# Kernel optimization log

Measured on AMD Instinct MI355X. Metric: run time of the kernel, lower is better.

Reference implementation:

```python
import jax, jax.numpy as jnp
import numpy as np

EMB = 1024
HEAD = 64


def setup_inputs() -> dict:
    key = jax.random.key(0)
    kx, kq, kk, kv = jax.random.split(key, 4)
    x = jax.random.normal(kx, (4, 4096, EMB), dtype=jnp.float32)
    # nn.Linear(emb, head, bias=False): y = x @ W^T; store transposed [emb, head]
    s = 1.0 / np.sqrt(EMB)
    Wq = jax.random.uniform(kq, (EMB, HEAD), jnp.float32, -s, s)
    Wk = jax.random.uniform(kk, (EMB, HEAD), jnp.float32, -s, s)
    Wv = jax.random.uniform(kv, (EMB, HEAD), jnp.float32, -s, s)
    return {"x": x, "Wq": Wq, "Wk": Wk, "Wv": Wv}


def reference(x, Wq, Wk, Wv):
    # x: [B, T, E]; projections -> [B, T, H]
    Q = jnp.einsum("bte,eh->bth", x, Wq)
    K = jnp.einsum("bte,eh->bth", x, Wk)
    V = jnp.einsum("bte,eh->bth", x, Wv)
    scale = 1.0 / np.sqrt(HEAD).astype(np.float32)
    scores = jnp.einsum("bqh,bkh->bqk", Q, K) * scale  # [B, T, T]
    attn = jax.nn.softmax(scores, axis=-1)
    out = jnp.einsum("bqk,bkh->bqh", attn, V)  # [B, T, H]
    return out
```

## Files before the change

### kernel.cpp

```cpp
#include <hip/hip_runtime.h>
#include <hip/hip_bf16.h>

typedef __bf16 bf16x8 __attribute__((ext_vector_type(8)));
typedef float floatx4 __attribute__((ext_vector_type(4)));

#define B_ 4
#define T_ 4096
#define E_ 1024
#define H_ 64
#define NSEG 8
#define SEGLEN (T_ / NSEG)
#define NROWS (B_ * T_)

#define QSCALE 0.18033688011112042f

#if __has_builtin(__builtin_amdgcn_exp2f)
#define EXP2(x) __builtin_amdgcn_exp2f(x)
#else
#define EXP2(x) exp2f(x)
#endif

__device__ __forceinline__ floatx4 mfma16(bf16x8 a, bf16x8 b, floatx4 c) {
  return __builtin_amdgcn_mfma_f32_16x16x32_bf16(a, b, c, 0, 0, 0);
}

#define GLDS16(gp, lp)                                                        \
  __builtin_amdgcn_global_load_lds(                                           \
      (const __attribute__((address_space(1))) void*)(gp),                    \
      (__attribute__((address_space(3))) void*)(lp), 16, 0, 0)

#define WAITCNT_VM(n) asm volatile("s_waitcnt vmcnt(" #n ")" ::: "memory")

__global__ void prep_wt_k(const float* __restrict__ Wq, const float* __restrict__ Wk,
                          const float* __restrict__ Wv, __bf16* __restrict__ Wfrag) {
  int gid = blockIdx.x * 4 + (threadIdx.x >> 6);
  int lane = threadIdx.x & 63;
  int ch = gid / 24, rem = gid % 24;
  int nt = rem >> 1, half = rem & 1;
  int g = lane >> 4, lm = lane & 15;
  int w = nt >> 2;
  const float* W = (w == 0) ? Wq : (w == 1) ? Wk : Wv;
  float sc = (w == 0) ? QSCALE : 1.0f;
  int h = (nt & 3) * 16 + lm;
  int e0 = ch * 64 + half * 32 + g * 8;
  __bf16* dst = Wfrag + (size_t)gid * 1024 / 2 + lane * 8;
  bf16x8 v;
#pragma unroll
  for (int j = 0; j < 8; j++) v[j] = (__bf16)(W[(size_t)(e0 + j) * H_ + h] * sc);
  *(bf16x8*)dst = v;
}

__global__ __launch_bounds__(64) void proj_k(
    const float* __restrict__ x, const __bf16* __restrict__ Wfrag,
    __bf16* __restrict__ Qo, __bf16* __restrict__ Ko, __bf16* __restrict__ Vt) {
  __shared__ __align__(16) char sX[4 * 4096];

  int lane = threadIdx.x;
  int lm = lane & 15, g = lane >> 4;
  int row_base = blockIdx.x * 16;

  const char* xb = (const char*)x;
  const char* wfb = (const char*)Wfrag + lane * 16;

  int srow = lane >> 4, sc = lane & 15;

#define STAGE_X(buf, ch)                                                      \
  _Pragma("unroll") for (int i = 0; i < 4; i++) {                             \
    int r = i * 4 + srow;                                                     \
    GLDS16(xb + (size_t)(row_base + r) * 4096 + (size_t)(ch) * 256 +          \
               ((sc ^ r) << 4),                                               \
           sX + (buf) * 4096 + i * 1024 + lane * 16);                         \
  }

  int aoff[2][2];
#pragma unroll
  for (int ks = 0; ks < 2; ks++) {
    int c0 = ks * 8 + g * 2;
    aoff[ks][0] = lm * 256 + ((c0 ^ lm) << 4);
    aoff[ks][1] = lm * 256 + (((c0 + 1) ^ lm) << 4);
  }

  floatx4 acc[12];
#pragma unroll
  for (int i = 0; i < 12; i++) acc[i] = (floatx4)0.0f;

  STAGE_X(0, 0);
  STAGE_X(1, 1);

#pragma unroll
  for (int ch = 0; ch < 16; ch++) {
    __builtin_amdgcn_sched_barrier(0);
    if (ch < 14) STAGE_X((ch + 2) & 3, ch + 2);
    __builtin_amdgcn_sched_barrier(0);
    if (ch < 14) {
      WAITCNT_VM(8);
    } else if (ch == 14) {
      WAITCNT_VM(4);
    } else {
      WAITCNT_VM(0);
    }
    __builtin_amdgcn_sched_barrier(0);

    const char* xB = sX + (ch & 3) * 4096;
    bf16x8 a[2];
#pragma unroll
    for (int ks = 0; ks < 2; ks++) {
      float4 f0 = *(const float4*)(xB + aoff[ks][0]);
      float4 f1 = *(const float4*)(xB + aoff[ks][1]);
      a[ks][0] = (__bf16)f0.x; a[ks][1] = (__bf16)f0.y;
      a[ks][2] = (__bf16)f0.z; a[ks][3] = (__bf16)f0.w;
      a[ks][4] = (__bf16)f1.x; a[ks][5] = (__bf16)f1.y;
      a[ks][6] = (__bf16)f1.z; a[ks][7] = (__bf16)f1.w;
    }

    const char* wp = wfb + (size_t)ch * 24576;
    bf16x8 wA[6], wB[6];
#pragma unroll
    for (int j = 0; j < 6; j++) wA[j] = *(const bf16x8*)(wp + (size_t)j * 2048);
#pragma unroll
    for (int j = 0; j < 6; j++) wB[j] = *(const bf16x8*)(wp + (size_t)(6 + j) * 2048);
#pragma unroll
    for (int j = 0; j < 6; j++) acc[j] = mfma16(a[0], wA[j], acc[j]);
#pragma unroll
    for (int j = 0; j < 6; j++) wA[j] = *(const bf16x8*)(wp + (size_t)j * 2048 + 1024);
#pragma unroll
    for (int j = 0; j < 6; j++) acc[6 + j] = mfma16(a[0], wB[j], acc[6 + j]);
#pragma unroll
    for (int j = 0; j < 6; j++)
      wB[j] = *(const bf16x8*)(wp + (size_t)(6 + j) * 2048 + 1024);
#pragma unroll
    for (int j = 0; j < 6; j++) acc[j] = mfma16(a[1], wA[j], acc[j]);
#pragma unroll
    for (int j = 0; j < 6; j++) acc[6 + j] = mfma16(a[1], wB[j], acc[6 + j]);
  }

#pragma unroll
  for (int nt = 0; nt < 12; nt++) {
    int w = nt >> 2;
    int h = (nt & 3) * 16 + lm;
#pragma unroll
    for (int r = 0; r < 4; r++) {
      __bf16 v = (__bf16)acc[nt][r];
      int rr = row_base + g * 4 + r;
      if (w == 0)      Qo[(size_t)rr * H_ + h] = v;
      else if (w == 1) Ko[(size_t)rr * H_ + h] = v;
      else {
        int b = rr >> 12, t = rr & (T_ - 1);
        int kin = t & 63;
        int pos = ((kin >> 5) << 5) + (((kin >> 2) & 3) << 3) +
                  (((kin >> 4) & 1) << 2) + (kin & 3);
        Vt[((size_t)b * H_ + h) * T_ + (t & ~63) + pos] = v;
      }
    }
  }
}

__global__ __launch_bounds__(256, 2) void attn_k(
    const __bf16* __restrict__ Q, const __bf16* __restrict__ K,
    const __bf16* __restrict__ Vt, __bf16* __restrict__ Op, float* __restrict__ lp) {
  __shared__ __align__(16) char sK[2 * 8192];
  __shared__ __align__(16) char sV[2 * 8192];

  int qb = blockIdx.x, b = blockIdx.y, seg = blockIdx.z;
  int tid = threadIdx.x, wv = tid >> 6, lane = tid & 63;
  int lm = lane & 15, g = lane >> 4;
  int q0 = qb * 256 + wv * 64;

  const __bf16* Qb = Q + (size_t)b * T_ * H_;
  const char* Kb = (const char*)(K + (size_t)b * T_ * H_);
  const char* Vb = (const char*)(Vt + (size_t)b * H_ * T_);

  bf16x8 qf[4][2];
#pragma unroll
  for (int qi = 0; qi < 4; qi++)
#pragma unroll
    for (int hs = 0; hs < 2; hs++)
      qf[qi][hs] =
          *(const bf16x8*)&Qb[(size_t)(q0 + qi * 16 + lm) * H_ + hs * 32 + g * 8];

  floatx4 o_acc[4][4], o_l[4];
#pragma unroll
  for (int qi = 0; qi < 4; qi++) {
#pragma unroll
    for (int i = 0; i < 4; i++) o_acc[qi][i] = (floatx4)0.0f;
    o_l[qi] = (floatx4)0.0f;
  }

  bf16x8 vone;
#pragma unroll
  for (int j = 0; j < 8; j++) vone[j] = (__bf16)1.0f;

  int s3 = lm & 7;
  int koff[4][2], voff[2][4];
#pragma unroll
  for (int mt = 0; mt < 4; mt++) {
    koff[mt][0] = (mt * 16 + lm) * 128 + ((g ^ s3) << 4);
    koff[mt][1] = (mt * 16 + lm) * 128 + (((g + 4) ^ s3) << 4);
  }
#pragma unroll
  for (int ks = 0; ks < 2; ks++)
#pragma unroll
    for (int nt = 0; nt < 4; nt++)
      voff[ks][nt] = (nt * 16 + lm) * 128 + (((ks * 4 + g) ^ s3) << 4);

  int srow = tid >> 3, schk = tid & 7;
  int swz0 = (schk ^ (srow & 7)) << 4;

#define ATTN_STAGE(buf, k0_)                                                  \
  {                                                                           \
    int off = (buf) * 8192 + tid * 16;                                        \
    GLDS16(Kb + (size_t)(k0_ + srow) * 128 + swz0, sK + off);                 \
    GLDS16(Kb + (size_t)(k0_ + srow + 32) * 128 + swz0, sK + off + 4096);     \
    GLDS16(Vb + (size_t)srow * (T_ * 2) + (size_t)(k0_) * 2 + swz0, sV + off);\
    GLDS16(Vb + (size_t)(srow + 32) * (T_ * 2) + (size_t)(k0_) * 2 + swz0,    \
           sV + off + 4096);                                                  \
  }

  int kbase = seg * SEGLEN;
  ATTN_STAGE(0, kbase);
  __syncthreads();

  for (int t = 0; t < SEGLEN / 64; t++) {
    if (t + 1 < SEGLEN / 64) ATTN_STAGE((t + 1) & 1, kbase + (t + 1) * 64);
    const char* kB = sK + (t & 1) * 8192;
    const char* vB = sV + (t & 1) * 8192;

    floatx4 s_acc[4][4];
#pragma unroll
    for (int mt = 0; mt < 4; mt++)
#pragma unroll
      for (int qi = 0; qi < 4; qi++) s_acc[mt][qi] = (floatx4)0.0f;
#pragma unroll
    for (int mt = 0; mt < 4; mt++) {
      bf16x8 a0 = *(const bf16x8*)(kB + koff[mt][0]);
      bf16x8 a1 = *(const bf16x8*)(kB + koff[mt][1]);
#pragma unroll
      for (int qi = 0; qi < 4; qi++) {
        s_acc[mt][qi] = mfma16(a0, qf[qi][0], s_acc[mt][qi]);
        s_acc[mt][qi] = mfma16(a1, qf[qi][1], s_acc[mt][qi]);
      }
    }

    bf16x8 pa[4][2];
#pragma unroll
    for (int qi = 0; qi < 4; qi++)
#pragma unroll
      for (int mt = 0; mt < 4; mt++)
#pragma unroll
        for (int r = 0; r < 4; r++)
          pa[qi][mt >> 1][(mt & 1) * 4 + r] = (__bf16)EXP2(s_acc[mt][qi][r]);

#pragma unroll
    for (int ks = 0; ks < 2; ks++) {
      bf16x8 bb[4];
#pragma unroll
      for (int nt = 0; nt < 4; nt++) bb[nt] = *(const bf16x8*)(vB + voff[ks][nt]);
#pragma unroll
      for (int qi = 0; qi < 4; qi++) {
#pragma unroll
        for (int nt = 0; nt < 4; nt++)
          o_acc[qi][nt] = mfma16(pa[qi][ks], bb[nt], o_acc[qi][nt]);
        o_l[qi] = mfma16(pa[qi][ks], vone, o_l[qi]);
      }
    }
    __syncthreads();
  }

  size_t rowbase = (size_t)seg * NROWS + (size_t)b * T_ + qb * 256 + wv * 64;
#pragma unroll
  for (int qi = 0; qi < 4; qi++) {
#pragma unroll
    for (int nt = 0; nt < 4; nt++)
#pragma unroll
      for (int r = 0; r < 4; r++)
        Op[(rowbase + qi * 16 + g * 4 + r) * 64 + nt * 16 + lm] =
            (__bf16)o_acc[qi][nt][r];
    if (lm == 0) {
#pragma unroll
      for (int r = 0; r < 4; r++)
        lp[rowbase + qi * 16 + g * 4 + r] = o_l[qi][r];
    }
  }
}

__global__ void combine_k(const __bf16* __restrict__ Op, const float* __restrict__ lp,
                          float* __restrict__ out) {
  int base = (blockIdx.x * 256 + threadIdx.x) * 8;
  int row = base >> 6;
  float L = 0.0f;
  float o[8];
#pragma unroll
  for (int j = 0; j < 8; j++) o[j] = 0.0f;
#pragma unroll
  for (int s = 0; s < NSEG; s++) {
    L += lp[(size_t)s * NROWS + row];
    bf16x8 v = *(const bf16x8*)&Op[(size_t)s * NROWS * 64 + base];
#pragma unroll
    for (int j = 0; j < 8; j++) o[j] += (float)v[j];
  }
  float inv = 1.0f / L;
  float4 r0 = {o[0] * inv, o[1] * inv, o[2] * inv, o[3] * inv};
  float4 r1 = {o[4] * inv, o[5] * inv, o[6] * inv, o[7] * inv};
  *(float4*)&out[base] = r0;
  *(float4*)&out[base + 4] = r1;
}

extern "C" void kernel_launch(void* const* d_in, const int* in_sizes, int n_in,
                              void* d_out, int out_size, void* d_ws, size_t ws_size,
                              hipStream_t stream) {
  const float* x  = (const float*)d_in[0];
  const float* Wq = (const float*)d_in[1];
  const float* Wk = (const float*)d_in[2];
  const float* Wv = (const float*)d_in[3];
  float* out = (float*)d_out;

  char* ws = (char*)d_ws;
  __bf16* Wf  = (__bf16*)(ws);
  __bf16* Qs  = (__bf16*)(ws + 0x60000);
  __bf16* Ks  = (__bf16*)(ws + 0x260000);
  __bf16* Vts = (__bf16*)(ws + 0x460000);
  __bf16* Op  = (__bf16*)(ws + 0x660000);
  float*  lp  = (float*)(ws + 0x1660000);

  prep_wt_k<<<96, 256, 0, stream>>>(Wq, Wk, Wv, Wf);
  proj_k<<<NROWS / 16, 64, 0, stream>>>(x, Wf, Qs, Ks, Vts);
  attn_k<<<dim3(T_ / 256, B_, NSEG), 256, 0, stream>>>(Qs, Ks, Vts, Op, lp);
  combine_k<<<NROWS * 64 / (256 * 8), 256, 0, stream>>>(Op, lp, out);
}
```

Measured before the change: 66.63 us.

## Split projection output columns across two waves and prefetch weights into registers

The projection kernel now runs 256-thread blocks where each wave handles a 16-row tile but only half of the 12 output column tiles (Q/K/V), so each row tile is processed by two waves. Each wave keeps a triple-buffered x stage in shared memory and prefetches the next chunk's weight fragments into registers after the current MFMAs. This doubles the number of waves for more parallelism and latency hiding, at the cost of loading x twice from global memory.

```diff
diff --git a/kernel.cpp b/kernel.cpp
--- a/kernel.cpp
+++ b/kernel.cpp
@@ -50,97 +50,92 @@
   *(bf16x8*)dst = v;
 }
 
-__global__ __launch_bounds__(64) void proj_k(
+__global__ __launch_bounds__(256) void proj_k(
     const float* __restrict__ x, const __bf16* __restrict__ Wfrag,
     __bf16* __restrict__ Qo, __bf16* __restrict__ Ko, __bf16* __restrict__ Vt) {
-  __shared__ __align__(16) char sX[4 * 4096];
-
-  int lane = threadIdx.x;
+  __shared__ __align__(16) char sX[4 * 12288];
+
+  int tid = threadIdx.x;
+  int wv = tid >> 6, lane = tid & 63;
   int lm = lane & 15, g = lane >> 4;
-  int row_base = blockIdx.x * 16;
+  int G = blockIdx.x * 4 + wv;
+  int rowjob = G >> 1, nth = G & 1;
+  int row_base = rowjob * 16;
 
   const char* xb = (const char*)x;
-  const char* wfb = (const char*)Wfrag + lane * 16;
-
-  int srow = lane >> 4, sc = lane & 15;
+  const char* wfb = (const char*)Wfrag + (size_t)(nth * 6 * 2) * 1024 + lane * 16;
+  char* sXw = sX + wv * 12288;
+
+  int srow_ = lane >> 4, spos_ = lane & 15;
 
 #define STAGE_X(buf, ch)                                                      \
   _Pragma("unroll") for (int i = 0; i < 4; i++) {                             \
-    int r = i * 4 + srow;                                                     \
+    int r = i * 4 + srow_;                                                    \
     GLDS16(xb + (size_t)(row_base + r) * 4096 + (size_t)(ch) * 256 +          \
-               ((sc ^ r) << 4),                                               \
-           sX + (buf) * 4096 + i * 1024 + lane * 16);                         \
-  }
-
-  int aoff[2][2];
-#pragma unroll
-  for (int ks = 0; ks < 2; ks++) {
-    int c0 = ks * 8 + g * 2;
-    aoff[ks][0] = lm * 256 + ((c0 ^ lm) << 4);
-    aoff[ks][1] = lm * 256 + (((c0 + 1) ^ lm) << 4);
-  }
-
-  floatx4 acc[12];
-#pragma unroll
-  for (int i = 0; i < 12; i++) acc[i] = (floatx4)0.0f;
+               ((spos_ ^ r) << 4),                                            \
+           sXw + (buf) * 4096 + i * 1024 + lane * 16);                        \
+  }
+
+  bf16x8 wreg[12];
+#define LOAD_W(ch)                                                            \
+  _Pragma("unroll") for (int j = 0; j < 12; j++)                              \
+      wreg[j] = *(const bf16x8*)(wfb + ((size_t)(ch) * 24 + j) * 1024);
+
+  floatx4 acc[6];
+#pragma unroll
+  for (int i = 0; i < 6; i++) acc[i] = (floatx4)0.0f;
 
   STAGE_X(0, 0);
+  __builtin_amdgcn_sched_barrier(0);
+  LOAD_W(0);
+  __builtin_amdgcn_sched_barrier(0);
   STAGE_X(1, 1);
+  __builtin_amdgcn_sched_barrier(0);
 
 #pragma unroll
   for (int ch = 0; ch < 16; ch++) {
-    __builtin_amdgcn_sched_barrier(0);
-    if (ch < 14) STAGE_X((ch + 2) & 3, ch + 2);
-    __builtin_amdgcn_sched_barrier(0);
-    if (ch < 14) {
-      WAITCNT_VM(8);
-    } else if (ch == 14) {
+    if (ch < 15) {
       WAITCNT_VM(4);
     } else {
       WAITCNT_VM(0);
     }
     __builtin_amdgcn_sched_barrier(0);
 
-    const char* xB = sX + (ch & 3) * 4096;
+    const char* xB = sXw + (ch % 3) * 4096;
     bf16x8 a[2];
 #pragma unroll
     for (int ks = 0; ks < 2; ks++) {
-      float4 f0 = *(const float4*)(xB + aoff[ks][0]);
-      float4 f1 = *(const float4*)(xB + aoff[ks][1]);
+      int c0 = ks * 8 + g * 2;
+      const char* xp = xB + lm * 256;
+      float4 f0 = *(const float4*)(xp + ((c0 ^ lm) << 4));
+      float4 f1 = *(const float4*)(xp + (((c0 + 1) ^ lm) << 4));
       a[ks][0] = (__bf16)f0.x; a[ks][1] = (__bf16)f0.y;
       a[ks][2] = (__bf16)f0.z; a[ks][3] = (__bf16)f0.w;
       a[ks][4] = (__bf16)f1.x; a[ks][5] = (__bf16)f1.y;
       a[ks][6] = (__bf16)f1.z; a[ks][7] = (__bf16)f1.w;
     }
 
-    const char* wp = wfb + (size_t)ch * 24576;
-    bf16x8 wA[6], wB[6];
-#pragma unroll
-    for (int j = 0; j < 6; j++) wA[j] = *(const bf16x8*)(wp + (size_t)j * 2048);
-#pragma unroll
-    for (int j = 0; j < 6; j++) wB[j] = *(const bf16x8*)(wp + (size_t)(6 + j) * 2048);
-#pragma unroll
-    for (int j = 0; j < 6; j++) acc[j] = mfma16(a[0], wA[j], acc[j]);
-#pragma unroll
-    for (int j = 0; j < 6; j++) wA[j] = *(const bf16x8*)(wp + (size_t)j * 2048 + 1024);
-#pragma unroll
-    for (int j = 0; j < 6; j++) acc[6 + j] = mfma16(a[0], wB[j], acc[6 + j]);
-#pragma unroll
-    for (int j = 0; j < 6; j++)
-      wB[j] = *(const bf16x8*)(wp + (size_t)(6 + j) * 2048 + 1024);
-#pragma unroll
-    for (int j = 0; j < 6; j++) acc[j] = mfma16(a[1], wA[j], acc[j]);
-#pragma unroll
-    for (int j = 0; j < 6; j++) acc[6 + j] = mfma16(a[1], wB[j], acc[6 + j]);
-  }
-
-#pragma unroll
-  for (int nt = 0; nt < 12; nt++) {
+#pragma unroll
+    for (int i = 0; i < 6; i++) {
+      acc[i] = mfma16(a[0], wreg[i * 2], acc[i]);
+      acc[i] = mfma16(a[1], wreg[i * 2 + 1], acc[i]);
+    }
+    __builtin_amdgcn_sched_barrier(0);
+
+    if (ch + 1 < 16) LOAD_W(ch + 1);
+    __builtin_amdgcn_sched_barrier(0);
+    if (ch + 2 < 16) STAGE_X((ch + 2) % 3, ch + 2);
+    __builtin_amdgcn_sched_barrier(0);
+  }
+
+#pragma unroll
+  for (int i = 0; i < 6; i++) {
+    int nt = nth * 6 + i;
     int w = nt >> 2;
     int h = (nt & 3) * 16 + lm;
 #pragma unroll
     for (int r = 0; r < 4; r++) {
-      __bf16 v = (__bf16)acc[nt][r];
+      __bf16 v = (__bf16)acc[i][r];
       int rr = row_base + g * 4 + r;
       if (w == 0)      Qo[(size_t)rr * H_ + h] = v;
       else if (w == 1) Ko[(size_t)rr * H_ + h] = v;
@@ -323,7 +318,7 @@
   float*  lp  = (float*)(ws + 0x1660000);
 
   prep_wt_k<<<96, 256, 0, stream>>>(Wq, Wk, Wv, Wf);
-  proj_k<<<NROWS / 16, 64, 0, stream>>>(x, Wf, Qs, Ks, Vts);
+  proj_k<<<NROWS / 32, 256, 0, stream>>>(x, Wf, Qs, Ks, Vts);
   attn_k<<<dim3(T_ / 256, B_, NSEG), 256, 0, stream>>>(Qs, Ks, Vts, Op, lp);
   combine_k<<<NROWS * 64 / (256 * 8), 256, 0, stream>>>(Op, lp, out);
 }
```

Measured after the change: 59.16 us. -11.2%, faster.
